# Kernel optimization log

Hardware: AMD Instinct MI355X
Metric: run time of the kernel (lower is better)

## Reference

```python
import jax, jax.numpy as jnp
import numpy as np

NUM_HEADS = 8
KS = 9  # kernel_size (square 9x9 neighborhood)


def _nearest_exact_resize(x, out_h, out_w):
    # PyTorch F.interpolate(mode='nearest-exact'): src = floor((i+0.5)*in/out)
    Hin, Win = x.shape[-2:]
    ih = jnp.clip(jnp.floor((jnp.arange(out_h) + 0.5) * (Hin / out_h)).astype(jnp.int32), 0, Hin - 1)
    iw = jnp.clip(jnp.floor((jnp.arange(out_w) + 0.5) * (Win / out_w)).astype(jnp.int32), 0, Win - 1)
    return x[:, :, ih[:, None], iw[None, :]]


def _window_indices(L, K, d):
    # NATTEN dilated neighborhood: positions split into residue classes mod d;
    # within each subgrid the K-wide window is clamped to stay in bounds.
    i = jnp.arange(L)
    r = i % d          # residue class
    ii = i // d        # index within subgrid
    Lr = (L - r + d - 1) // d  # subgrid length for this residue
    start = jnp.clip(ii - K // 2, 0, Lr - K)
    taps = jnp.arange(K)
    return r[:, None] + d * (start[:, None] + taps[None, :])  # [L, K]


def _cross_attention(q, k, v):
    B, C, Hq, Wq = q.shape
    Hk, Wk = k.shape[-2:]
    n = NUM_HEADS
    dh = C // n
    scale = dh ** -0.5
    # dilation logic from forward()
    raw_dh = Hq // max(Hk, 1)
    raw_dw = Wq // max(Wk, 1)
    max_dh = max(Hq // KS, 1)
    max_dw = max(Wq // KS, 1)
    dil_h = min(max(raw_dh, 1), max_dh)
    dil_w = min(max(raw_dw, 1), max_dw)
    # resize k, v to query resolution (nearest-exact)
    kr = _nearest_exact_resize(k, Hq, Wq)
    vr = _nearest_exact_resize(v, Hq, Wq)
    # b (n d) h w -> b h w n d
    to_bhwnd = lambda x: x.reshape(B, n, dh, Hq, Wq).transpose(0, 3, 4, 1, 2)
    qh, kh, vh = to_bhwnd(q), to_bhwnd(kr), to_bhwnd(vr)
    hid = _window_indices(Hq, KS, dil_h)  # [Hq, K]
    wid = _window_indices(Wq, KS, dil_w)  # [Wq, K]
    # gather local K/V windows -> [B, Hq, Wq, K, K, n, dh]
    kw = kh[:, hid[:, None, :, None], wid[None, :, None, :]]
    vw = vh[:, hid[:, None, :, None], wid[None, :, None, :]]
    kw = kw.reshape(B, Hq, Wq, KS * KS, n, dh)
    vw = vw.reshape(B, Hq, Wq, KS * KS, n, dh)
    scores = jnp.einsum('bhwnd,bhwknd->bhwnk', qh, kw) * scale
    wts = jax.nn.softmax(scores, axis=-1)
    out = jnp.einsum('bhwnk,bhwknd->bhwnd', wts, vw)
    # b h w n d -> b (n d) h w
    return out.transpose(0, 3, 4, 1, 2).reshape(B, C, Hq, Wq)


def setup_inputs() -> dict:
    key = jax.random.key(0)
    kq, kk, kv = jax.random.split(key, 3)
    q = jax.random.normal(kq, (2, 512, 48, 48), dtype=jnp.float32)
    k = jax.random.normal(kk, (2, 512, 24, 24), dtype=jnp.float32)
    v = jax.random.normal(kv, (2, 512, 24, 24), dtype=jnp.float32)
    return {"q": q, "k": k, "v": v}


def reference(q, k, v):
    return _cross_attention(q, k, v)
```

## Files before the change

### kernel.cpp

```cpp
#include <hip/hip_runtime.h>

typedef short bf16x8 __attribute__((ext_vector_type(8)));
typedef float f32x4 __attribute__((ext_vector_type(4)));
typedef ushort u16x8 __attribute__((ext_vector_type(8)));

#define MFMA16(A, B, C) __builtin_amdgcn_mfma_f32_16x16x32_bf16((A), (B), (C), 0, 0, 0)

static __device__ __forceinline__ ushort f2bf(float f) {
    unsigned u = __builtin_bit_cast(unsigned, f);
    unsigned r = (u + 0x7FFFu + ((u >> 16) & 1u)) >> 16;
    return (ushort)r;
}
static __device__ __forceinline__ unsigned pk2(float a, float b) {
    return (unsigned)f2bf(a) | ((unsigned)f2bf(b) << 16);
}
static __device__ __forceinline__ bf16x8 ldg8(const ushort* p) {
    uint4 u = *(const uint4*)p;
    return __builtin_bit_cast(bf16x8, u);
}

#define OFF_KT 0
#define OFF_V4 1572864
#define WS_NEED 8126464

__global__ __launch_bounds__(256) void prep(const float* __restrict__ k,
                                            const float* __restrict__ v,
                                            ushort* __restrict__ kt,
                                            ushort* __restrict__ v4) {
    __shared__ float tile[32][33];
    int bid = blockIdx.x;

    if (bid < 576) {
        int b = bid / 288;
        int rem = bid % 288;
        int p0 = (rem / 16) * 32;
        int c0 = (rem % 16) * 32;
        int tx = threadIdx.x & 31, tw = threadIdx.x >> 5;
#pragma unroll
        for (int i = 0; i < 4; ++i) {
            int r = tw + i * 8;
            tile[r][tx] = k[(size_t)(b * 512 + c0 + r) * 576 + p0 + tx];
        }
        __syncthreads();
#pragma unroll
        for (int i = 0; i < 4; ++i) {
            int r = tw + i * 8;
            int pix = p0 + r;
            int kr = pix / 24, kc = pix % 24;
            kt[((size_t)(b * 24 + kr) * 32 + kc) * 512 + c0 + tx] = f2bf(tile[tx][r]);
        }
    } else {
        int tid = (bid - 576) * 256 + threadIdx.x;
        int col0 = (tid & 3) * 8;
        int rowlin = tid >> 2;
        int kr = rowlin % 25;
        int c = (rowlin / 25) % 512;
        int b = (rowlin / (25 * 512)) & 1;
        int s = rowlin / (25 * 512 * 2);
        const float* src = v + (size_t)(b * 512 + c) * 576 + kr * 24;
        u16x8 w;
#pragma unroll
        for (int j = 0; j < 8; ++j) {
            int srcc = col0 + j + 2 * s;
            w[j] = (kr < 24 && srcc < 24) ? f2bf(src[srcc]) : (ushort)0;
        }
        *(u16x8*)&v4[(size_t)rowlin * 32 + col0] = w;
    }
}

__global__ __launch_bounds__(64) void attn(const float* __restrict__ q,
                                           const ushort* __restrict__ kt,
                                           const ushort* __restrict__ v4,
                                           float* __restrict__ out) {
    __shared__ __align__(16) unsigned Plds[16][84];

    int bid = blockIdx.x;
    int h = bid & 7;
    int t = bid >> 3;
    int tx = t % 6;
    int tyb = t / 6;
    int ty = tyb % 24;
    int b = tyb / 24;

    int l = threadIdx.x;
    int pix = l & 15, g = l >> 4;
    int px = pix & 7, py = pix >> 3;
    int y = ty * 2 + py, x = tx * 8 + px;

    int sr = min(max(ty - 4, 0), 15);
    int sw0 = min(max(4 * tx - 4, 0), 15);
    int swe = sw0 & ~1;
    int sw = min(max((x >> 1) - 4, 0), 15);
    int dx = sw - swe;
    int s2 = swe & 6, scopy = s2 >> 1, colbase = swe - s2;

    const float* qsrc = q + (size_t)(b * 512 + h * 64 + g * 8) * 2304 + y * 48 + x;
    float t0[8], t1[8];
#pragma unroll
    for (int j = 0; j < 8; ++j) t0[j] = qsrc[(size_t)j * 2304];
#pragma unroll
    for (int j = 0; j < 8; ++j) t1[j] = qsrc[(size_t)(j + 32) * 2304];
    bf16x8 q0, q1;
#pragma unroll
    for (int j = 0; j < 8; ++j) {
        q0[j] = (short)f2bf(t0[j]);
        q1[j] = (short)f2bf(t1[j]);
    }

    f32x4 sc[9];
#pragma unroll
    for (int m = 0; m < 9; ++m) {
        int koff = (((b * 24 + sr + m) << 5) + swe + pix) * 512 + h * 64 + g * 8;
        bf16x8 k0 = ldg8(kt + koff), k1 = ldg8(kt + koff + 32);
        f32x4 a = {0.f, 0.f, 0.f, 0.f};
        a = MFMA16(k0, q0, a);
        a = MFMA16(k1, q1, a);
        sc[m] = a;
    }

    const float C2 = 0.18033688011112042f;
    float mx = -3.0e38f;
#pragma unroll
    for (int r = 0; r < 4; ++r) {
        if ((unsigned)(g * 4 + r - dx) <= 8u) {
#pragma unroll
            for (int m = 0; m < 9; ++m) mx = fmaxf(mx, sc[m][r]);
        }
    }
    mx = fmaxf(mx, __shfl_xor(mx, 16));
    mx = fmaxf(mx, __shfl_xor(mx, 32));
    float sum = 0.f;
#pragma unroll
    for (int m = 0; m < 9; ++m) {
#pragma unroll
        for (int r = 0; r < 4; ++r) {
            bool valid = (unsigned)(g * 4 + r - dx) <= 8u;
            float p = valid ? exp2f((sc[m][r] - mx) * C2) : 0.f;
            sc[m][r] = p;
            sum += p;
        }
    }
    sum += __shfl_xor(sum, 16);
    sum += __shfl_xor(sum, 32);

#pragma unroll
    for (int m = 0; m < 9; ++m) {
        uint2 w;
        w.x = pk2(sc[m][0], sc[m][1]);
        w.y = pk2(sc[m][2], sc[m][3]);
        *(uint2*)&Plds[pix][m * 8 + g * 2] = w;
    }
    *(uint2*)&Plds[pix][72 + g * 2] = make_uint2(0u, 0u);

    f32x4 o[4] = {{0.f, 0.f, 0.f, 0.f}, {0.f, 0.f, 0.f, 0.f}, {0.f, 0.f, 0.f, 0.f}, {0.f, 0.f, 0.f, 0.f}};
#pragma unroll
    for (int ks = 0; ks < 5; ++ks) {
        uint4 pw = *(const uint4*)&Plds[pix][ks * 16 + g * 4];
        bf16x8 pf = __builtin_bit_cast(bf16x8, pw);
        int tap0 = ks * 32 + g * 8;
        int tr = tap0 >> 4, tc0 = tap0 & 15;
#pragma unroll
        for (int md = 0; md < 4; ++md) {
            int c = h * 64 + md * 16 + pix;
            const ushort* vp = v4 + ((size_t)((scopy * 2 + b) * 512 + c) * 25 + sr + tr) * 32 + colbase + tc0;
            o[md] = MFMA16(ldg8(vp), pf, o[md]);
        }
    }

    float invd = 1.0f / sum;
#pragma unroll
    for (int md = 0; md < 4; ++md) {
#pragma unroll
        for (int r = 0; r < 4; ++r) {
            int d = md * 16 + g * 4 + r;
            out[((size_t)(b * 512 + h * 64 + d) * 48 + y) * 48 + x] = o[md][r] * invd;
        }
    }
}

extern "C" void kernel_launch(void* const* d_in, const int* in_sizes, int n_in,
                              void* d_out, int out_size, void* d_ws, size_t ws_size,
                              hipStream_t stream) {
    const float* q = (const float*)d_in[0];
    const float* k = (const float*)d_in[1];
    const float* v = (const float*)d_in[2];
    float* out = (float*)d_out;
    char* ws = (char*)d_ws;
    if (ws_size < (size_t)WS_NEED) return;

    ushort* kt = (ushort*)(ws + OFF_KT);
    ushort* v4 = (ushort*)(ws + OFF_V4);

    prep<<<2176, 256, 0, stream>>>(k, v, kt, v4);
    attn<<<2304, 64, 0, stream>>>(q, kt, v4, out);
}
```

Baseline: 24.19 us.

## Split attention block across two wavefronts with LDS score reduction

The attention block grows from one wavefront to two. Each wave computes a partial QK score over half the head dimension, and the partial scores are summed through shared memory. Wave 0 alone does the softmax and writes normalized probabilities to LDS, then each wave runs the PV MFMAs for half of the output channels. This is meant to give more memory-level parallelism and fewer serial loads per wave, at the cost of an extra LDS exchange, two block barriers and an idle wave during the softmax.

```diff
diff --git a/kernel.cpp b/kernel.cpp
--- a/kernel.cpp
+++ b/kernel.cpp
@@ -68,10 +68,11 @@
     }
 }
 
-__global__ __launch_bounds__(64) void attn(const float* __restrict__ q,
-                                           const ushort* __restrict__ kt,
-                                           const ushort* __restrict__ v4,
-                                           float* __restrict__ out) {
+__global__ __launch_bounds__(128) void attn(const float* __restrict__ q,
+                                            const ushort* __restrict__ kt,
+                                            const ushort* __restrict__ v4,
+                                            float* __restrict__ out) {
+    __shared__ float Xch[36][64];
     __shared__ __align__(16) unsigned Plds[16][84];
 
     int bid = blockIdx.x;
@@ -82,7 +83,8 @@
     int ty = tyb % 24;
     int b = tyb / 24;
 
-    int l = threadIdx.x;
+    int l = threadIdx.x & 63;
+    int w = threadIdx.x >> 6;
     int pix = l & 15, g = l >> 4;
     int px = pix & 7, py = pix >> 3;
     int y = ty * 2 + py, x = tx * 8 + px;
@@ -94,65 +96,75 @@
     int dx = sw - swe;
     int s2 = swe & 6, scopy = s2 >> 1, colbase = swe - s2;
 
-    const float* qsrc = q + (size_t)(b * 512 + h * 64 + g * 8) * 2304 + y * 48 + x;
-    float t0[8], t1[8];
+    const float* qsrc = q + (size_t)(b * 512 + h * 64 + w * 32 + g * 8) * 2304 + y * 48 + x;
+    float t0[8];
 #pragma unroll
     for (int j = 0; j < 8; ++j) t0[j] = qsrc[(size_t)j * 2304];
-#pragma unroll
-    for (int j = 0; j < 8; ++j) t1[j] = qsrc[(size_t)(j + 32) * 2304];
-    bf16x8 q0, q1;
-#pragma unroll
-    for (int j = 0; j < 8; ++j) {
-        q0[j] = (short)f2bf(t0[j]);
-        q1[j] = (short)f2bf(t1[j]);
-    }
+    bf16x8 q0;
+#pragma unroll
+    for (int j = 0; j < 8; ++j) q0[j] = (short)f2bf(t0[j]);
 
     f32x4 sc[9];
 #pragma unroll
     for (int m = 0; m < 9; ++m) {
-        int koff = (((b * 24 + sr + m) << 5) + swe + pix) * 512 + h * 64 + g * 8;
-        bf16x8 k0 = ldg8(kt + koff), k1 = ldg8(kt + koff + 32);
+        int koff = (((b * 24 + sr + m) << 5) + swe + pix) * 512 + h * 64 + w * 32 + g * 8;
         f32x4 a = {0.f, 0.f, 0.f, 0.f};
-        a = MFMA16(k0, q0, a);
-        a = MFMA16(k1, q1, a);
+        a = MFMA16(ldg8(kt + koff), q0, a);
         sc[m] = a;
     }
 
-    const float C2 = 0.18033688011112042f;
-    float mx = -3.0e38f;
-#pragma unroll
-    for (int r = 0; r < 4; ++r) {
-        if ((unsigned)(g * 4 + r - dx) <= 8u) {
-#pragma unroll
-            for (int m = 0; m < 9; ++m) mx = fmaxf(mx, sc[m][r]);
-        }
-    }
-    mx = fmaxf(mx, __shfl_xor(mx, 16));
-    mx = fmaxf(mx, __shfl_xor(mx, 32));
-    float sum = 0.f;
-#pragma unroll
-    for (int m = 0; m < 9; ++m) {
+    if (w == 1) {
+#pragma unroll
+        for (int m = 0; m < 9; ++m) {
+#pragma unroll
+            for (int r = 0; r < 4; ++r) Xch[m * 4 + r][l] = sc[m][r];
+        }
+    }
+    __syncthreads();
+
+    if (w == 0) {
+#pragma unroll
+        for (int m = 0; m < 9; ++m) {
+#pragma unroll
+            for (int r = 0; r < 4; ++r) sc[m][r] += Xch[m * 4 + r][l];
+        }
+        const float C2 = 0.18033688011112042f;
+        float mx = -3.0e38f;
 #pragma unroll
         for (int r = 0; r < 4; ++r) {
-            bool valid = (unsigned)(g * 4 + r - dx) <= 8u;
-            float p = valid ? exp2f((sc[m][r] - mx) * C2) : 0.f;
-            sc[m][r] = p;
-            sum += p;
-        }
-    }
-    sum += __shfl_xor(sum, 16);
-    sum += __shfl_xor(sum, 32);
-
-#pragma unroll
-    for (int m = 0; m < 9; ++m) {
-        uint2 w;
-        w.x = pk2(sc[m][0], sc[m][1]);
-        w.y = pk2(sc[m][2], sc[m][3]);
-        *(uint2*)&Plds[pix][m * 8 + g * 2] = w;
-    }
-    *(uint2*)&Plds[pix][72 + g * 2] = make_uint2(0u, 0u);
-
-    f32x4 o[4] = {{0.f, 0.f, 0.f, 0.f}, {0.f, 0.f, 0.f, 0.f}, {0.f, 0.f, 0.f, 0.f}, {0.f, 0.f, 0.f, 0.f}};
+            if ((unsigned)(g * 4 + r - dx) <= 8u) {
+#pragma unroll
+                for (int m = 0; m < 9; ++m) mx = fmaxf(mx, sc[m][r]);
+            }
+        }
+        mx = fmaxf(mx, __shfl_xor(mx, 16));
+        mx = fmaxf(mx, __shfl_xor(mx, 32));
+        float sum = 0.f;
+#pragma unroll
+        for (int m = 0; m < 9; ++m) {
+#pragma unroll
+            for (int r = 0; r < 4; ++r) {
+                bool valid = (unsigned)(g * 4 + r - dx) <= 8u;
+                float p = valid ? exp2f((sc[m][r] - mx) * C2) : 0.f;
+                sc[m][r] = p;
+                sum += p;
+            }
+        }
+        sum += __shfl_xor(sum, 16);
+        sum += __shfl_xor(sum, 32);
+        float invd = 1.0f / sum;
+#pragma unroll
+        for (int m = 0; m < 9; ++m) {
+            uint2 pw;
+            pw.x = pk2(sc[m][0] * invd, sc[m][1] * invd);
+            pw.y = pk2(sc[m][2] * invd, sc[m][3] * invd);
+            *(uint2*)&Plds[pix][m * 8 + g * 2] = pw;
+        }
+        *(uint2*)&Plds[pix][72 + g * 2] = make_uint2(0u, 0u);
+    }
+    __syncthreads();
+
+    f32x4 o[2] = {{0.f, 0.f, 0.f, 0.f}, {0.f, 0.f, 0.f, 0.f}};
 #pragma unroll
     for (int ks = 0; ks < 5; ++ks) {
         uint4 pw = *(const uint4*)&Plds[pix][ks * 16 + g * 4];
@@ -160,20 +172,19 @@
         int tap0 = ks * 32 + g * 8;
         int tr = tap0 >> 4, tc0 = tap0 & 15;
 #pragma unroll
-        for (int md = 0; md < 4; ++md) {
-            int c = h * 64 + md * 16 + pix;
+        for (int i = 0; i < 2; ++i) {
+            int c = h * 64 + (2 * w + i) * 16 + pix;
             const ushort* vp = v4 + ((size_t)((scopy * 2 + b) * 512 + c) * 25 + sr + tr) * 32 + colbase + tc0;
-            o[md] = MFMA16(ldg8(vp), pf, o[md]);
-        }
-    }
-
-    float invd = 1.0f / sum;
-#pragma unroll
-    for (int md = 0; md < 4; ++md) {
+            o[i] = MFMA16(ldg8(vp), pf, o[i]);
+        }
+    }
+
+#pragma unroll
+    for (int i = 0; i < 2; ++i) {
 #pragma unroll
         for (int r = 0; r < 4; ++r) {
-            int d = md * 16 + g * 4 + r;
-            out[((size_t)(b * 512 + h * 64 + d) * 48 + y) * 48 + x] = o[md][r] * invd;
+            int d = (2 * w + i) * 16 + g * 4 + r;
+            out[((size_t)(b * 512 + h * 64 + d) * 48 + y) * 48 + x] = o[i][r];
         }
     }
 }
@@ -192,5 +203,5 @@
     ushort* v4 = (ushort*)(ws + OFF_V4);
 
     prep<<<2176, 256, 0, stream>>>(k, v, kt, v4);
-    attn<<<2304, 64, 0, stream>>>(q, kt, v4, out);
-}
+    attn<<<2304, 128, 0, stream>>>(q, kt, v4, out);
+}
```

Measured after the change: 25.71 us. 1.06x slower.

## Fuse K/V prep and attention into one cooperative kernel with grid sync

Applied to the files above, without the earlier changes.

Replaces the two-kernel prep+attention sequence with a single cooperative launch. Each block first issues its Q gather, then does a slice of the K transpose/bf16 conversion and the V shifted-copy build, and then waits on a grid-wide barrier before running the attention body. The aim is to drop one kernel launch boundary and overlap Q loads with the prep work. In exchange it adds a grid sync, host-side occupancy queries on every call, and a requirement that all 2304 blocks be co-resident, with the old two-kernel path kept as a fallback.

```diff
diff --git a/kernel.cpp b/kernel.cpp
--- a/kernel.cpp
+++ b/kernel.cpp
@@ -1,4 +1,5 @@
 #include <hip/hip_runtime.h>
+#include <hip/hip_cooperative_groups.h>
 
 typedef short bf16x8 __attribute__((ext_vector_type(8)));
 typedef float f32x4 __attribute__((ext_vector_type(4)));
@@ -22,6 +23,128 @@
 #define OFF_KT 0
 #define OFF_V4 1572864
 #define WS_NEED 8126464
+
+struct TileCtx {
+    int h, tx, ty, b;
+    int pix, g, y, x;
+    int sr, swe, dx, scopy, colbase;
+};
+
+static __device__ __forceinline__ TileCtx make_ctx(int job, int l) {
+    TileCtx c;
+    c.h = job & 7;
+    int t = job >> 3;
+    c.tx = t % 6;
+    int tyb = t / 6;
+    c.ty = tyb % 24;
+    c.b = tyb / 24;
+    c.pix = l & 15;
+    c.g = l >> 4;
+    int px = c.pix & 7, py = c.pix >> 3;
+    c.y = c.ty * 2 + py;
+    c.x = c.tx * 8 + px;
+    c.sr = min(max(c.ty - 4, 0), 15);
+    int sw0 = min(max(4 * c.tx - 4, 0), 15);
+    c.swe = sw0 & ~1;
+    int sw = min(max((c.x >> 1) - 4, 0), 15);
+    c.dx = sw - c.swe;
+    int s2 = c.swe & 6;
+    c.scopy = s2 >> 1;
+    c.colbase = c.swe - s2;
+    return c;
+}
+
+static __device__ __forceinline__ void q_gather(const float* __restrict__ q,
+                                                const TileCtx& c, bf16x8& q0, bf16x8& q1) {
+    const float* qsrc = q + (size_t)(c.b * 512 + c.h * 64 + c.g * 8) * 2304 + c.y * 48 + c.x;
+    float t0[8], t1[8];
+#pragma unroll
+    for (int j = 0; j < 8; ++j) t0[j] = qsrc[(size_t)j * 2304];
+#pragma unroll
+    for (int j = 0; j < 8; ++j) t1[j] = qsrc[(size_t)(j + 32) * 2304];
+#pragma unroll
+    for (int j = 0; j < 8; ++j) {
+        q0[j] = (short)f2bf(t0[j]);
+        q1[j] = (short)f2bf(t1[j]);
+    }
+}
+
+static __device__ __forceinline__ void attn_body(const TileCtx& c, bf16x8 q0, bf16x8 q1,
+                                                 const ushort* __restrict__ kt,
+                                                 const ushort* __restrict__ v4,
+                                                 float* __restrict__ out,
+                                                 unsigned (*Plds)[84]) {
+    int pix = c.pix, g = c.g;
+    f32x4 sc[9];
+#pragma unroll
+    for (int m = 0; m < 9; ++m) {
+        int koff = (((c.b * 24 + c.sr + m) << 5) + c.swe + pix) * 512 + c.h * 64 + g * 8;
+        bf16x8 k0 = ldg8(kt + koff), k1 = ldg8(kt + koff + 32);
+        f32x4 a = {0.f, 0.f, 0.f, 0.f};
+        a = MFMA16(k0, q0, a);
+        a = MFMA16(k1, q1, a);
+        sc[m] = a;
+    }
+
+    const float C2 = 0.18033688011112042f;
+    float mx = -3.0e38f;
+#pragma unroll
+    for (int r = 0; r < 4; ++r) {
+        if ((unsigned)(g * 4 + r - c.dx) <= 8u) {
+#pragma unroll
+            for (int m = 0; m < 9; ++m) mx = fmaxf(mx, sc[m][r]);
+        }
+    }
+    mx = fmaxf(mx, __shfl_xor(mx, 16));
+    mx = fmaxf(mx, __shfl_xor(mx, 32));
+    float sum = 0.f;
+#pragma unroll
+    for (int m = 0; m < 9; ++m) {
+#pragma unroll
+        for (int r = 0; r < 4; ++r) {
+            bool valid = (unsigned)(g * 4 + r - c.dx) <= 8u;
+            float p = valid ? exp2f((sc[m][r] - mx) * C2) : 0.f;
+            sc[m][r] = p;
+            sum += p;
+        }
+    }
+    sum += __shfl_xor(sum, 16);
+    sum += __shfl_xor(sum, 32);
+
+#pragma unroll
+    for (int m = 0; m < 9; ++m) {
+        uint2 w;
+        w.x = pk2(sc[m][0], sc[m][1]);
+        w.y = pk2(sc[m][2], sc[m][3]);
+        *(uint2*)&Plds[pix][m * 8 + g * 2] = w;
+    }
+    *(uint2*)&Plds[pix][72 + g * 2] = make_uint2(0u, 0u);
+
+    f32x4 o[4] = {{0.f, 0.f, 0.f, 0.f}, {0.f, 0.f, 0.f, 0.f}, {0.f, 0.f, 0.f, 0.f}, {0.f, 0.f, 0.f, 0.f}};
+#pragma unroll
+    for (int ks = 0; ks < 5; ++ks) {
+        uint4 pw = *(const uint4*)&Plds[pix][ks * 16 + g * 4];
+        bf16x8 pf = __builtin_bit_cast(bf16x8, pw);
+        int tap0 = ks * 32 + g * 8;
+        int tr = tap0 >> 4, tc0 = tap0 & 15;
+#pragma unroll
+        for (int md = 0; md < 4; ++md) {
+            int ch = c.h * 64 + md * 16 + pix;
+            const ushort* vp = v4 + ((size_t)((c.scopy * 2 + c.b) * 512 + ch) * 25 + c.sr + tr) * 32 + c.colbase + tc0;
+            o[md] = MFMA16(ldg8(vp), pf, o[md]);
+        }
+    }
+
+    float invd = 1.0f / sum;
+#pragma unroll
+    for (int md = 0; md < 4; ++md) {
+#pragma unroll
+        for (int r = 0; r < 4; ++r) {
+            int d = md * 16 + g * 4 + r;
+            out[((size_t)(c.b * 512 + c.h * 64 + d) * 48 + c.y) * 48 + c.x] = o[md][r] * invd;
+        }
+    }
+}
 
 __global__ __launch_bounds__(256) void prep(const float* __restrict__ k,
                                             const float* __restrict__ v,
@@ -73,109 +196,68 @@
                                            const ushort* __restrict__ v4,
                                            float* __restrict__ out) {
     __shared__ __align__(16) unsigned Plds[16][84];
+    TileCtx c = make_ctx(blockIdx.x, threadIdx.x);
+    bf16x8 q0, q1;
+    q_gather(q, c, q0, q1);
+    attn_body(c, q0, q1, kt, v4, out, Plds);
+}
+
+__global__ __launch_bounds__(64, 4) void fused(const float* __restrict__ q,
+                                               const float* __restrict__ k,
+                                               const float* __restrict__ v,
+                                               ushort* __restrict__ kt,
+                                               ushort* __restrict__ v4,
+                                               float* __restrict__ out) {
+    __shared__ __align__(16) unsigned Plds[16][84];
 
     int bid = blockIdx.x;
-    int h = bid & 7;
-    int t = bid >> 3;
-    int tx = t % 6;
-    int tyb = t / 6;
-    int ty = tyb % 24;
-    int b = tyb / 24;
-
     int l = threadIdx.x;
-    int pix = l & 15, g = l >> 4;
-    int px = pix & 7, py = pix >> 3;
-    int y = ty * 2 + py, x = tx * 8 + px;
-
-    int sr = min(max(ty - 4, 0), 15);
-    int sw0 = min(max(4 * tx - 4, 0), 15);
-    int swe = sw0 & ~1;
-    int sw = min(max((x >> 1) - 4, 0), 15);
-    int dx = sw - swe;
-    int s2 = swe & 6, scopy = s2 >> 1, colbase = swe - s2;
-
-    const float* qsrc = q + (size_t)(b * 512 + h * 64 + g * 8) * 2304 + y * 48 + x;
-    float t0[8], t1[8];
-#pragma unroll
-    for (int j = 0; j < 8; ++j) t0[j] = qsrc[(size_t)j * 2304];
-#pragma unroll
-    for (int j = 0; j < 8; ++j) t1[j] = qsrc[(size_t)(j + 32) * 2304];
+    TileCtx c = make_ctx(bid, l);
+
     bf16x8 q0, q1;
-#pragma unroll
-    for (int j = 0; j < 8; ++j) {
-        q0[j] = (short)f2bf(t0[j]);
-        q1[j] = (short)f2bf(t1[j]);
-    }
-
-    f32x4 sc[9];
-#pragma unroll
-    for (int m = 0; m < 9; ++m) {
-        int koff = (((b * 24 + sr + m) << 5) + swe + pix) * 512 + h * 64 + g * 8;
-        bf16x8 k0 = ldg8(kt + koff), k1 = ldg8(kt + koff + 32);
-        f32x4 a = {0.f, 0.f, 0.f, 0.f};
-        a = MFMA16(k0, q0, a);
-        a = MFMA16(k1, q1, a);
-        sc[m] = a;
-    }
-
-    const float C2 = 0.18033688011112042f;
-    float mx = -3.0e38f;
-#pragma unroll
-    for (int r = 0; r < 4; ++r) {
-        if ((unsigned)(g * 4 + r - dx) <= 8u) {
-#pragma unroll
-            for (int m = 0; m < 9; ++m) mx = fmaxf(mx, sc[m][r]);
-        }
-    }
-    mx = fmaxf(mx, __shfl_xor(mx, 16));
-    mx = fmaxf(mx, __shfl_xor(mx, 32));
-    float sum = 0.f;
-#pragma unroll
-    for (int m = 0; m < 9; ++m) {
-#pragma unroll
-        for (int r = 0; r < 4; ++r) {
-            bool valid = (unsigned)(g * 4 + r - dx) <= 8u;
-            float p = valid ? exp2f((sc[m][r] - mx) * C2) : 0.f;
-            sc[m][r] = p;
-            sum += p;
-        }
-    }
-    sum += __shfl_xor(sum, 16);
-    sum += __shfl_xor(sum, 32);
-
-#pragma unroll
-    for (int m = 0; m < 9; ++m) {
-        uint2 w;
-        w.x = pk2(sc[m][0], sc[m][1]);
-        w.y = pk2(sc[m][2], sc[m][3]);
-        *(uint2*)&Plds[pix][m * 8 + g * 2] = w;
-    }
-    *(uint2*)&Plds[pix][72 + g * 2] = make_uint2(0u, 0u);
-
-    f32x4 o[4] = {{0.f, 0.f, 0.f, 0.f}, {0.f, 0.f, 0.f, 0.f}, {0.f, 0.f, 0.f, 0.f}, {0.f, 0.f, 0.f, 0.f}};
-#pragma unroll
-    for (int ks = 0; ks < 5; ++ks) {
-        uint4 pw = *(const uint4*)&Plds[pix][ks * 16 + g * 4];
-        bf16x8 pf = __builtin_bit_cast(bf16x8, pw);
-        int tap0 = ks * 32 + g * 8;
-        int tr = tap0 >> 4, tc0 = tap0 & 15;
-#pragma unroll
-        for (int md = 0; md < 4; ++md) {
-            int c = h * 64 + md * 16 + pix;
-            const ushort* vp = v4 + ((size_t)((scopy * 2 + b) * 512 + c) * 25 + sr + tr) * 32 + colbase + tc0;
-            o[md] = MFMA16(ldg8(vp), pf, o[md]);
-        }
-    }
-
-    float invd = 1.0f / sum;
-#pragma unroll
-    for (int md = 0; md < 4; ++md) {
-#pragma unroll
-        for (int r = 0; r < 4; ++r) {
-            int d = md * 16 + g * 4 + r;
-            out[((size_t)(b * 512 + h * 64 + d) * 48 + y) * 48 + x] = o[md][r] * invd;
-        }
-    }
+    q_gather(q, c, q0, q1);
+
+    int tid = bid * 64 + l;
+    {
+        int c0 = (tid & 127) * 4;
+        int pixlin = tid >> 7;
+        int kb = pixlin / 576;
+        int rem = pixlin % 576;
+        int kr = rem / 24, kc = rem % 24;
+        const float* kp = k + (size_t)(kb * 512 + c0) * 576 + kr * 24 + kc;
+        ushort4 w;
+        w.x = f2bf(kp[0]);
+        w.y = f2bf(kp[576]);
+        w.z = f2bf(kp[1152]);
+        w.w = f2bf(kp[1728]);
+        *(ushort4*)&kt[((size_t)(kb * 24 + kr) * 32 + kc) * 512 + c0] = w;
+    }
+#pragma unroll
+    for (int i = 0; i < 3; ++i) {
+        int gid = tid + i * 147456;
+        if (gid < 409600) {
+            int col0 = (gid & 3) * 8;
+            int rowlin = gid >> 2;
+            int kr = rowlin % 25;
+            int ch = (rowlin / 25) % 512;
+            int vb = (rowlin / (25 * 512)) & 1;
+            int s = rowlin / (25 * 512 * 2);
+            const float* src = v + (size_t)(vb * 512 + ch) * 576 + kr * 24;
+            u16x8 w;
+#pragma unroll
+            for (int j = 0; j < 8; ++j) {
+                int srcc = col0 + j + 2 * s;
+                w[j] = (kr < 24 && srcc < 24) ? f2bf(src[srcc]) : (ushort)0;
+            }
+            *(u16x8*)&v4[(size_t)rowlin * 32 + col0] = w;
+        }
+    }
+
+    __threadfence();
+    cooperative_groups::this_grid().sync();
+    __threadfence();
+
+    attn_body(c, q0, q1, kt, v4, out, Plds);
 }
 
 extern "C" void kernel_launch(void* const* d_in, const int* in_sizes, int n_in,
@@ -191,6 +273,19 @@
     ushort* kt = (ushort*)(ws + OFF_KT);
     ushort* v4 = (ushort*)(ws + OFF_V4);
 
+    int dev = 0;
+    (void)hipGetDevice(&dev);
+    int numCU = 0;
+    (void)hipDeviceGetAttribute(&numCU, hipDeviceAttributeMultiprocessorCount, dev);
+    int maxBlocksPerCU = 0;
+    (void)hipOccupancyMaxActiveBlocksPerMultiprocessor(&maxBlocksPerCU, (const void*)fused, 64, 0);
+
+    bool coop_ok = (numCU > 0) && ((long)maxBlocksPerCU * numCU >= 2304);
+    if (coop_ok) {
+        void* args[] = {(void*)&q, (void*)&k, (void*)&v, (void*)&kt, (void*)&v4, (void*)&out};
+        hipError_t rc = hipLaunchCooperativeKernel((const void*)fused, dim3(2304), dim3(64), args, 0, stream);
+        if (rc == hipSuccess) return;
+    }
     prep<<<2176, 256, 0, stream>>>(k, v, kt, v4);
     attn<<<2304, 64, 0, stream>>>(q, kt, v4, out);
 }
```

Measured after the change: 24.28 us. About the same (+0.4%).

## Pre-swizzle K and V into MFMA fragment order for contiguous wave loads

Applied to the files above, without the earlier changes.

The prep kernel now writes K and V into layouts arranged exactly in the per-lane MFMA operand order. K is replicated for each of five column-window starts, and V for each shift/column-block combination. As a result, each lane in the attention kernel reads a contiguous 16-byte chunk indexed by lane id, so a wave's loads are fully coalesced instead of strided gathers. The cost is a larger workspace and more prep blocks and writes, and the K transpose no longer goes through shared memory, so its reads are strided.

```diff
diff --git a/kernel.cpp b/kernel.cpp
--- a/kernel.cpp
+++ b/kernel.cpp
@@ -19,58 +19,69 @@
     return __builtin_bit_cast(bf16x8, u);
 }
 
-#define OFF_KT 0
-#define OFF_V4 1572864
-#define WS_NEED 8126464
+#define OFF_KT5 0
+#define OFF_V5  3932160
+#define WS_NEED 16515072
 
 __global__ __launch_bounds__(256) void prep(const float* __restrict__ k,
                                             const float* __restrict__ v,
-                                            ushort* __restrict__ kt,
-                                            ushort* __restrict__ v4) {
-    __shared__ float tile[32][33];
+                                            ushort* __restrict__ kt5,
+                                            ushort* __restrict__ v5) {
     int bid = blockIdx.x;
-
-    if (bid < 576) {
-        int b = bid / 288;
-        int rem = bid % 288;
-        int p0 = (rem / 16) * 32;
-        int c0 = (rem % 16) * 32;
-        int tx = threadIdx.x & 31, tw = threadIdx.x >> 5;
-#pragma unroll
-        for (int i = 0; i < 4; ++i) {
-            int r = tw + i * 8;
-            tile[r][tx] = k[(size_t)(b * 512 + c0 + r) * 576 + p0 + tx];
-        }
-        __syncthreads();
-#pragma unroll
-        for (int i = 0; i < 4; ++i) {
-            int r = tw + i * 8;
-            int pix = p0 + r;
-            int kr = pix / 24, kc = pix % 24;
-            kt[((size_t)(b * 24 + kr) * 32 + kc) * 512 + c0 + tx] = f2bf(tile[tx][r]);
-        }
+    if (bid < 960) {
+        int tid = bid * 256 + threadIdx.x;
+        int pix = tid & 15;
+        int g = (tid >> 4) & 3;
+        int h = (tid >> 6) & 7;
+        int kk = (tid >> 9) & 1;
+        int X = tid >> 10;
+        int krow = X % 24;
+        int Z = X / 24;
+        int si = Z % 5, b = Z / 5;
+        const int swetab[5] = {0, 4, 8, 12, 14};
+        int col = swetab[si] + pix;
+        u16x8 w;
+        if (col < 24) {
+            const float* kp = k + (size_t)(b * 512 + h * 64 + kk * 32 + g * 8) * 576 + krow * 24 + col;
+#pragma unroll
+            for (int j = 0; j < 8; ++j) w[j] = f2bf(kp[(size_t)j * 576]);
+        } else {
+#pragma unroll
+            for (int j = 0; j < 8; ++j) w[j] = 0;
+        }
+        *(u16x8*)&kt5[(size_t)tid * 8] = w;
     } else {
-        int tid = (bid - 576) * 256 + threadIdx.x;
-        int col0 = (tid & 3) * 8;
-        int rowlin = tid >> 2;
-        int kr = rowlin % 25;
-        int c = (rowlin / 25) % 512;
-        int b = (rowlin / (25 * 512)) & 1;
-        int s = rowlin / (25 * 512 * 2);
-        const float* src = v + (size_t)(b * 512 + c) * 576 + kr * 24;
+        int tid = (bid - 960) * 256 + threadIdx.x;
+        int pix = tid & 15;
+        int g = (tid >> 4) & 3;
+        int Y = tid >> 6;
+        int r0 = Y % 24;
+        int Y1 = Y / 24;
+        int md = Y1 & 3;
+        int Y2 = Y1 >> 2;
+        int h = Y2 & 7;
+        int Y3 = Y2 >> 3;
+        int cb8 = Y3 & 1;
+        int Y4 = Y3 >> 1;
+        int vb = Y4 & 1;
+        int s = Y4 >> 1;
+        int row = r0 + (g >> 1);
+        int c0 = cb8 * 8 + 8 * (g & 1) + 2 * s;
+        int ch = h * 64 + md * 16 + pix;
+        const float* vp = v + (size_t)(vb * 512 + ch) * 576 + row * 24;
         u16x8 w;
 #pragma unroll
         for (int j = 0; j < 8; ++j) {
-            int srcc = col0 + j + 2 * s;
-            w[j] = (kr < 24 && srcc < 24) ? f2bf(src[srcc]) : (ushort)0;
-        }
-        *(u16x8*)&v4[(size_t)rowlin * 32 + col0] = w;
+            int cc = c0 + j;
+            w[j] = (row < 24 && cc < 24) ? f2bf(vp[cc]) : (ushort)0;
+        }
+        *(u16x8*)&v5[(size_t)tid * 8] = w;
     }
 }
 
 __global__ __launch_bounds__(64) void attn(const float* __restrict__ q,
-                                           const ushort* __restrict__ kt,
-                                           const ushort* __restrict__ v4,
+                                           const ushort* __restrict__ kt5,
+                                           const ushort* __restrict__ v5,
                                            float* __restrict__ out) {
     __shared__ __align__(16) unsigned Plds[16][84];
 
@@ -93,6 +104,8 @@
     int sw = min(max((x >> 1) - 4, 0), 15);
     int dx = sw - swe;
     int s2 = swe & 6, scopy = s2 >> 1, colbase = swe - s2;
+    int si = (swe + 2) >> 2;
+    int cb8 = colbase >> 3;
 
     const float* qsrc = q + (size_t)(b * 512 + h * 64 + g * 8) * 2304 + y * 48 + x;
     float t0[8], t1[8];
@@ -108,10 +121,12 @@
     }
 
     f32x4 sc[9];
+    const size_t kfixed = (size_t)(b * 5 + si) * 24;
 #pragma unroll
     for (int m = 0; m < 9; ++m) {
-        int koff = (((b * 24 + sr + m) << 5) + swe + pix) * 512 + h * 64 + g * 8;
-        bf16x8 k0 = ldg8(kt + koff), k1 = ldg8(kt + koff + 32);
+        size_t kb = (((kfixed + sr + m) * 2) * 8 + h) * 512 + l * 8;
+        bf16x8 k0 = ldg8(kt5 + kb);
+        bf16x8 k1 = ldg8(kt5 + kb + 4096);
         f32x4 a = {0.f, 0.f, 0.f, 0.f};
         a = MFMA16(k0, q0, a);
         a = MFMA16(k1, q1, a);
@@ -153,16 +168,15 @@
     *(uint2*)&Plds[pix][72 + g * 2] = make_uint2(0u, 0u);
 
     f32x4 o[4] = {{0.f, 0.f, 0.f, 0.f}, {0.f, 0.f, 0.f, 0.f}, {0.f, 0.f, 0.f, 0.f}, {0.f, 0.f, 0.f, 0.f}};
+    const size_t vfixed = ((((size_t)scopy * 2 + b) * 2 + cb8) * 8 + h) * 4;
 #pragma unroll
     for (int ks = 0; ks < 5; ++ks) {
         uint4 pw = *(const uint4*)&Plds[pix][ks * 16 + g * 4];
         bf16x8 pf = __builtin_bit_cast(bf16x8, pw);
-        int tap0 = ks * 32 + g * 8;
-        int tr = tap0 >> 4, tc0 = tap0 & 15;
+        int r0 = sr + 2 * ks;
 #pragma unroll
         for (int md = 0; md < 4; ++md) {
-            int c = h * 64 + md * 16 + pix;
-            const ushort* vp = v4 + ((size_t)((scopy * 2 + b) * 512 + c) * 25 + sr + tr) * 32 + colbase + tc0;
+            const ushort* vp = v5 + ((vfixed + md) * 24 + r0) * 512 + l * 8;
             o[md] = MFMA16(ldg8(vp), pf, o[md]);
         }
     }
@@ -188,9 +202,9 @@
     char* ws = (char*)d_ws;
     if (ws_size < (size_t)WS_NEED) return;
 
-    ushort* kt = (ushort*)(ws + OFF_KT);
-    ushort* v4 = (ushort*)(ws + OFF_V4);
-
-    prep<<<2176, 256, 0, stream>>>(k, v, kt, v4);
-    attn<<<2304, 64, 0, stream>>>(q, kt, v4, out);
-}
+    ushort* kt5 = (ushort*)(ws + OFF_KT5);
+    ushort* v5 = (ushort*)(ws + OFF_V5);
+
+    prep<<<4032, 256, 0, stream>>>(k, v, kt5, v5);
+    attn<<<2304, 64, 0, stream>>>(q, kt5, v5, out);
+}
```

New measurement: 32.78 us. 35.5% more time.
